# Performance work log

Measured on AMD Instinct MI355X. Metric: run time of the kernel, lower is better.

The kernel has to match this reference:

```python
import jax, jax.numpy as jnp
import numpy as np

N = 50000        # n_nodes
E = 1_600_000    # n_edges (avg degree 32)
IN = 128         # in_dim
H = 8            # num_heads
R = 16           # hidden_rank
D = 16           # out_dim (per head)
SCALE = float(np.sqrt(D))


def setup_inputs() -> dict:
    key = jax.random.key(0)
    k1, k2, k3, k4, k5, k6 = jax.random.split(key, 6)
    h = jax.random.normal(k1, (N, IN), jnp.float32)
    src = jax.random.randint(k2, (E,), 0, N, dtype=jnp.int32)
    dst = jax.random.randint(k3, (E,), 0, N, dtype=jnp.int32)
    s = 1.0 / np.sqrt(IN)  # kaiming-ish scale
    p = jax.random.normal(k4, (IN, H * R), jnp.float32) * s
    q = jax.random.normal(k5, (IN, H * R), jnp.float32) * s
    Wv = jax.random.normal(k6, (IN, H * D), jnp.float32) * s
    return {"h": h, "src": src, "dst": dst, "p": p, "q": q, "Wv": Wv}


def reference(h, src, dst, p, q, Wv):
    # global_attention_type == 'transform' -> atted = h
    K = (h @ q).reshape(N, H, R)   # K_h = atted @ _q
    Q = (h @ p).reshape(N, H, R)   # Q_h = h @ _p
    V = (h @ Wv).reshape(N, H, D)  # V_h = V(h), no bias
    # per-edge score: (K[src] * Q[dst]).sum(-1, keepdim), then scaled exp
    score = jnp.sum(K[src] * Q[dst], axis=-1, keepdims=True)   # [E, H, 1]
    score = jnp.exp(jnp.clip(score / SCALE, -5.0, 5.0))
    # scatter-sum into destination nodes
    wV = jax.ops.segment_sum(V[src] * score, dst, num_segments=N)  # [N, H, D]
    z = jax.ops.segment_sum(score, dst, num_segments=N)            # [N, H, 1]
    z = jnp.where(z == 0, jnp.float32(0.001), z)
    return wV / z
```

## Files before the change

### kernel.cpp

```cpp
#include <hip/hip_runtime.h>
#include <hip/hip_fp16.h>


#define HNODE 64
#define EPB   4096
#define BKT_SHIFT 7
#define BKT_CAP 5120
#define CHUNK 40

typedef _Float16 f16x8 __attribute__((ext_vector_type(8)));
typedef float    f32x4 __attribute__((ext_vector_type(4)));
typedef _Float16 hv2   __attribute__((ext_vector_type(2)));

__device__ __forceinline__ float fdot2(unsigned a, unsigned b, float c) {
#if __has_builtin(__builtin_amdgcn_fdot2)
    return __builtin_amdgcn_fdot2(__builtin_bit_cast(hv2, a),
                                  __builtin_bit_cast(hv2, b), c, false);
#else
    __half2 ah = *(__half2*)&a, bh = *(__half2*)&b;
    float2 af = __half22float2(ah), bf = __half22float2(bh);
    return c + af.x * bf.x + af.y * bf.y;
#endif
}

__device__ __forceinline__ float2 h2f(unsigned u) {
    __half2 hh = *(__half2*)&u;
    return __half22float2(hh);
}

__device__ __forceinline__ unsigned pack2(float a, float b) {
    __half2 hh = __floats2half2_rn(a, b);
    return *(unsigned*)&hh;
}

__device__ __forceinline__ float clamp5(float x) {
#if __has_builtin(__builtin_amdgcn_fmed3f)
    return __builtin_amdgcn_fmed3f(x, -5.f, 5.f);
#else
    return fminf(fmaxf(x, -5.f), 5.f);
#endif
}

#if __has_builtin(__builtin_amdgcn_mov_dpp)
#define QBCAST(v, J) __builtin_amdgcn_mov_dpp((v), (J) * 0x55, 0xF, 0xF, true)
__device__ __forceinline__ float qadd_xor1(float x) {
    int y = __builtin_amdgcn_mov_dpp(__float_as_int(x), 0xB1, 0xF, 0xF, true);
    return x + __int_as_float(y);
}
__device__ __forceinline__ float qadd_xor2(float x) {
    int y = __builtin_amdgcn_mov_dpp(__float_as_int(x), 0x4E, 0xF, 0xF, true);
    return x + __int_as_float(y);
}
#else
#define QBCAST(v, J) __shfl((v), ((threadIdx.x & 63) & ~3) + (J), 64)
__device__ __forceinline__ float qadd_xor1(float x) { return x + __shfl_xor(x, 1); }
__device__ __forceinline__ float qadd_xor2(float x) { return x + __shfl_xor(x, 2); }
#endif

__global__ __launch_bounds__(256) void wt_convert_kernel(
    const float* __restrict__ Wq, const float* __restrict__ Wp,
    const float* __restrict__ Wv, __half* __restrict__ Wt)
{
    int o = blockIdx.x * 256 + threadIdx.x;
    int m = o >> 14, rem = o & 16383;
    int nn = rem >> 7, kk = rem & 127;
    const float* W = (m == 0) ? Wq : (m == 1) ? Wp : Wv;
    Wt[o] = __float2half(W[kk * 128 + nn]);
}

__global__ __launch_bounds__(256) void gemm_scatter_kernel(
    const float* __restrict__ h, const __half* __restrict__ Wt,
    unsigned* __restrict__ KV, __half* __restrict__ Q, int n,
    const int* __restrict__ src, const int* __restrict__ dst,
    unsigned* __restrict__ ebuf, int* __restrict__ cnts,
    int E, int nbkt, int nblk_e, int gemm_blocks)
{
    __shared__ __align__(16) char smem[39936];
    const int t = threadIdx.x;

    if ((int)blockIdx.x < gemm_blocks) {
        _Float16* ws = (_Float16*)smem;
        const int wid = t >> 6, lane = t & 63;
        const int node0 = blockIdx.x * HNODE;
        const int mrow = lane & 15, quad = lane >> 4;

        const int row = node0 + wid * 16 + mrow;
        const bool rowvalid = (row < n);
        const int rowc = rowvalid ? row : (n - 1);

        f16x8 hfr[4];
        #pragma unroll
        for (int s = 0; s < 4; s++) {
            const float4* hp = (const float4*)(h + (size_t)rowc * 128 + quad * 8 + 32 * s);
            float4 f0 = hp[0], f1 = hp[1];
            f16x8 a;
            a[0] = (_Float16)f0.x; a[1] = (_Float16)f0.y;
            a[2] = (_Float16)f0.z; a[3] = (_Float16)f0.w;
            a[4] = (_Float16)f1.x; a[5] = (_Float16)f1.y;
            a[6] = (_Float16)f1.z; a[7] = (_Float16)f1.w;
            hfr[s] = a;
        }

        f32x4 acc[3][8];
        #pragma unroll
        for (int m = 0; m < 3; m++)
            #pragma unroll
            for (int ct = 0; ct < 8; ct++) acc[m][ct] = (f32x4){0.f, 0.f, 0.f, 0.f};

        #pragma unroll
        for (int m = 0; m < 3; m++) {
            __syncthreads();
            {
                const uint4* wg = (const uint4*)(Wt + (size_t)m * 16384);
                #pragma unroll
                for (int i = 0; i < 8; i++) {
                    int idx = t * 8 + i;
                    int r = idx >> 4, seg = idx & 15;
                    *(uint4*)(ws + r * 136 + seg * 8) = wg[idx];
                }
            }
            __syncthreads();
            #pragma unroll
            for (int s = 0; s < 4; s++) {
                #pragma unroll
                for (int ct = 0; ct < 8; ct++) {
                    f16x8 a = *(const f16x8*)(ws + (ct * 16 + mrow) * 136 + quad * 8 + 32 * s);
                    acc[m][ct] = __builtin_amdgcn_mfma_f32_16x16x32_f16(a, hfr[s], acc[m][ct], 0, 0, 0);
                }
            }
        }

        if (rowvalid) {
            #pragma unroll
            for (int ct = 0; ct < 8; ct++) {
                uint4 ov;
                ov.x = pack2(acc[0][ct][0], acc[0][ct][1]);
                ov.y = pack2(acc[0][ct][2], acc[0][ct][3]);
                ov.z = pack2(acc[2][ct][0], acc[2][ct][1]);
                ov.w = pack2(acc[2][ct][2], acc[2][ct][3]);
                *(uint4*)(KV + (((size_t)ct * n + row) << 4) + 4 * quad) = ov;
                uint2 qv;
                qv.x = pack2(acc[1][ct][0], acc[1][ct][1]);
                qv.y = pack2(acc[1][ct][2], acc[1][ct][3]);
                *(uint2*)(Q + (((size_t)ct * n + row) << 4) + 4 * quad) = qv;
            }
        }
    } else {
        unsigned long long* sorted = (unsigned long long*)smem;
        int* cnt  = (int*)(smem + 32768);
        int* lofs = (int*)(smem + 34816);
        int* ts   = (int*)(smem + 36864);
        int* tot_sh = (int*)(smem + 37888);

        int blk = blockIdx.x - gemm_blocks;
        for (int i = t; i < 512; i += 256) cnt[i] = 0;
        __syncthreads();

        int4 sv[4], dv[4], rk[4];
        int base = blk * EPB + t * 4;
        #pragma unroll
        for (int r = 0; r < 4; r++) {
            int i = base + r * 1024;
            if (i + 3 < E) {
                sv[r] = *(const int4*)(src + i);
                dv[r] = *(const int4*)(dst + i);
            } else {
                int tsrc[4], tdst[4];
                for (int k = 0; k < 4; k++) {
                    int j = i + k;
                    tsrc[k] = (j < E) ? src[j] : 0;
                    tdst[k] = (j < E) ? dst[j] : -1;
                }
                sv[r] = make_int4(tsrc[0], tsrc[1], tsrc[2], tsrc[3]);
                dv[r] = make_int4(tdst[0], tdst[1], tdst[2], tdst[3]);
            }
            rk[r].x = (dv[r].x >= 0) ? atomicAdd(&cnt[dv[r].x >> BKT_SHIFT], 1) : 0;
            rk[r].y = (dv[r].y >= 0) ? atomicAdd(&cnt[dv[r].y >> BKT_SHIFT], 1) : 0;
            rk[r].z = (dv[r].z >= 0) ? atomicAdd(&cnt[dv[r].z >> BKT_SHIFT], 1) : 0;
            rk[r].w = (dv[r].w >= 0) ? atomicAdd(&cnt[dv[r].w >> BKT_SHIFT], 1) : 0;
        }
        __syncthreads();

        for (int i = t; i < nbkt; i += 256)
            cnts[blk * 512 + i] = cnt[i];

        int c0 = cnt[2 * t], c1 = cnt[2 * t + 1];
        int ps = c0 + c1;
        ts[t] = ps; __syncthreads();
        for (int off = 1; off < 256; off <<= 1) {
            int x = ts[t];
            int y = (t >= off) ? ts[t - off] : 0;
            __syncthreads();
            ts[t] = x + y;
            __syncthreads();
        }
        int pbase = ts[t] - ps;
        lofs[2 * t] = pbase;
        lofs[2 * t + 1] = pbase + c0;
        if (t == 255) *tot_sh = ts[255];
        __syncthreads();

        #pragma unroll
        for (int r = 0; r < 4; r++) {
            int s, d;
            d = dv[r].x; if (d >= 0) { s = sv[r].x; sorted[lofs[d >> BKT_SHIFT] + rk[r].x] = ((unsigned long long)d << 18) | (unsigned)s; }
            d = dv[r].y; if (d >= 0) { s = sv[r].y; sorted[lofs[d >> BKT_SHIFT] + rk[r].y] = ((unsigned long long)d << 18) | (unsigned)s; }
            d = dv[r].z; if (d >= 0) { s = sv[r].z; sorted[lofs[d >> BKT_SHIFT] + rk[r].z] = ((unsigned long long)d << 18) | (unsigned)s; }
            d = dv[r].w; if (d >= 0) { s = sv[r].w; sorted[lofs[d >> BKT_SHIFT] + rk[r].w] = ((unsigned long long)d << 18) | (unsigned)s; }
        }
        __syncthreads();

        int tot = *tot_sh;
        #pragma unroll
        for (int j = 0; j < 16; j++) {
            int i = j * 256 + t;
            if (i < tot) {
                unsigned long long e = sorted[i];
                int d = (int)(e >> 18);
                int b = d >> BKT_SHIFT;
                int k = i - lofs[b];
                if (k < CHUNK)
                    ebuf[((size_t)b * nblk_e + blk) * CHUNK + k] =
                        ((unsigned)(d & 127) << 18) | (unsigned)(e & 0x3FFFFu);
            }
        }
    }
}

__global__ __launch_bounds__(512) void fine_scatter_kernel(
    const unsigned* __restrict__ ebuf, const int* __restrict__ cnts,
    int2* __restrict__ offs, unsigned short* __restrict__ csr,
    int* __restrict__ nodeord, int N, int nblk_e, int nbkt)
{
    __shared__ int cval[512];
    __shared__ int cofs[512];
    __shared__ int ts[512];
    __shared__ int ldeg[128];
    __shared__ int lstart[129];
    __shared__ int tot_sh;
    __shared__ unsigned sedge[BKT_CAP];
    __shared__ unsigned short srank[BKT_CAP];
    __shared__ int lcsr[BKT_CAP];

    int b = blockIdx.x, t = threadIdx.x;
    int node_base = b << BKT_SHIFT;
    int seg0 = b * BKT_CAP;

    int c = (t < nblk_e) ? cnts[t * 512 + b] : 0;
    if (c > CHUNK) c = CHUNK;
    cval[t] = c;
    ts[t] = c;
    if (t < 128) ldeg[t] = 0;
    __syncthreads();
    for (int off = 1; off < 512; off <<= 1) {
        int x = ts[t];
        int y = (t >= off) ? ts[t - off] : 0;
        __syncthreads();
        ts[t] = x + y;
        __syncthreads();
    }
    cofs[t] = ts[t] - cval[t];
    if (t == 511) tot_sh = (ts[511] <= BKT_CAP) ? ts[511] : BKT_CAP;
    __syncthreads();

    for (int idx = t; idx < nblk_e * CHUNK; idx += 512) {
        int cc = idx / CHUNK, k = idx - cc * CHUNK;
        if (k < cval[cc]) {
            int pos = cofs[cc] + k;
            if (pos < BKT_CAP)
                sedge[pos] = ebuf[((size_t)b * nblk_e + cc) * CHUNK + k];
        }
    }
    __syncthreads();

    int tot = tot_sh;
    for (int i = t; i < tot; i += 512)
        srank[i] = (unsigned short)atomicAdd(&ldeg[sedge[i] >> 18], 1);
    __syncthreads();

    int mydeg = (t < 128) ? ldeg[t] : 0;
    if (t < 128) ts[t] = mydeg;
    __syncthreads();
    for (int off = 1; off < 128; off <<= 1) {
        int x = (t < 128) ? ts[t] : 0;
        int y = (t >= off && t < 128) ? ts[t - off] : 0;
        __syncthreads();
        if (t < 128) ts[t] = x + y;
        __syncthreads();
    }
    if (t < 128) {
        int lbeg = ts[t] - mydeg;
        lstart[t] = lbeg;
        int node = node_base + t;
        if (node < N) offs[node] = make_int2(seg0 + lbeg, seg0 + lbeg + mydeg);
    }
    if (t == 127) lstart[128] = ts[127];
    __syncthreads();

    if (t < 128) {
        int dt = ldeg[t];
        int r = 0;
        for (int j = 0; j < 128; j++) {
            int dj = ldeg[j];
            r += (int)((dj > dt) || (dj == dt && j < t));
        }
        nodeord[(b << 7) + r] = t;
    }

    for (int i = t; i < tot; i += 512) {
        unsigned v = sedge[i];
        lcsr[lstart[v >> 18] + srank[i]] = (int)(v & 0x3FFFFu);
    }
    __syncthreads();

    for (int i = t; i < tot; i += 512)
        csr[seg0 + i] = (unsigned short)lcsr[i];
}

#define AGG_COMPUTE(A, J)                                                      \
    {                                                                          \
        float s = fdot2(A.x, qq.x, fdot2(A.y, qq.y, 0.f));                     \
        s = qadd_xor1(s);                                                      \
        s = qadd_xor2(s);                                                      \
        float xx = clamp5(s * 0.25f);                                          \
        float sc = (e + (J) < cnt) ? __expf(xx) : 0.f;                         \
        accz += sc;                                                            \
        float2 v0 = h2f(A.z), v1 = h2f(A.w);                                   \
        av0 += sc * v0.x; av1 += sc * v0.y;                                    \
        av2 += sc * v1.x; av3 += sc * v1.y;                                    \
    }

__global__ __launch_bounds__(256) void aggregate_kernel(
    const unsigned* __restrict__ KVh,
    const uint2* __restrict__ Qr,
    const int2* __restrict__ offs, const unsigned short* __restrict__ csr,
    const int* __restrict__ nodeord,
    float* __restrict__ out, int n)
{
    const int t = threadIdx.x;
    const int head = blockIdx.x & 7;
    const int rest = blockIdx.x >> 3;
    const int bkt = rest >> 1, sub = rest & 1;
    const int lane = t & 63;
    const int g = lane >> 2;
    const int p = lane & 3;
    const int chunk = ((t >> 6) << 1) | sub;

    const int spos = (bkt << 7) + (chunk << 4) + g;
    const int local = nodeord[spos];
    const int node = (bkt << 7) + local;
    const bool nvalid = (node < n);
    const int nodec = nvalid ? node : 0;

    int beg = 0, cnt = 0;
    if (nvalid) {
        int2 be = offs[node];
        beg = be.x; cnt = be.y - be.x;
    }

    const size_t hn = (size_t)head * n;
    const uint2 qq = Qr[(hn + nodec) * 4 + p];
    const char* kvb = (const char*)KVh + hn * 64;
    const unsigned ppo = (unsigned)p << 4;

    float accz = 0.f;
    float av0 = 0.f, av1 = 0.f, av2 = 0.f, av3 = 0.f;

    const int cl = (cnt > 0) ? (cnt - 1) : 0;

    int np = (p < cl) ? p : cl;
    int idxA = (int)csr[beg + np];
    uint4 a0, a1, a2, a3;
    {
        unsigned j;
        j = (unsigned)QBCAST(idxA, 0); a0 = *(const uint4*)(kvb + ((j << 6) | ppo));
        j = (unsigned)QBCAST(idxA, 1); a1 = *(const uint4*)(kvb + ((j << 6) | ppo));
        j = (unsigned)QBCAST(idxA, 2); a2 = *(const uint4*)(kvb + ((j << 6) | ppo));
        j = (unsigned)QBCAST(idxA, 3); a3 = *(const uint4*)(kvb + ((j << 6) | ppo));
    }
    np = 4 + p; np = (np < cl) ? np : cl;
    int idxB = (int)csr[beg + np];

    for (int e = 0; e < cnt; e += 4) {
        unsigned j;
        uint4 b0, b1, b2, b3;
        j = (unsigned)QBCAST(idxB, 0); b0 = *(const uint4*)(kvb + ((j << 6) | ppo));
        j = (unsigned)QBCAST(idxB, 1); b1 = *(const uint4*)(kvb + ((j << 6) | ppo));
        j = (unsigned)QBCAST(idxB, 2); b2 = *(const uint4*)(kvb + ((j << 6) | ppo));
        j = (unsigned)QBCAST(idxB, 3); b3 = *(const uint4*)(kvb + ((j << 6) | ppo));
        np = e + 8 + p; np = (np < cl) ? np : cl;
        idxB = (int)csr[beg + np];

        AGG_COMPUTE(a0, 0)
        AGG_COMPUTE(a1, 1)
        AGG_COMPUTE(a2, 2)
        AGG_COMPUTE(a3, 3)

        a0 = b0; a1 = b1; a2 = b2; a3 = b3;
    }

    if (nvalid) {
        float z = accz;
        if (z == 0.f) z = 0.001f;
        float inv = 1.0f / z;
        *(float4*)(out + (size_t)node * 128 + head * 16 + p * 4) =
            make_float4(av0 * inv, av1 * inv, av2 * inv, av3 * inv);
    }
}


extern "C" void kernel_launch(void* const* d_in, const int* in_sizes, int n_in,
                              void* d_out, int out_size, void* d_ws, size_t ws_size,
                              hipStream_t stream)
{
    const float* h   = (const float*)d_in[0];
    const int*   src = (const int*)d_in[1];
    const int*   dst = (const int*)d_in[2];
    const float* p   = (const float*)d_in[3];
    const float* q   = (const float*)d_in[4];
    const float* wv  = (const float*)d_in[5];
    float* out = (float*)d_out;

    const int N = in_sizes[0] / 128;
    const int E = in_sizes[1];
    const int nbkt = (N + 127) >> BKT_SHIFT;
    const int nblk_e = (E + EPB - 1) / EPB;
    const int gemm_blocks = (N + HNODE - 1) / HNODE;

    unsigned* KV = (unsigned*)d_ws;
    __half* Qh   = (__half*)(KV + (size_t)N * 128);
    unsigned* ebuf = (unsigned*)(Qh + (size_t)N * 128);
    int* cnts    = (int*)(ebuf + (size_t)nbkt * nblk_e * CHUNK);
    unsigned short* csr16 = (unsigned short*)(cnts + (size_t)nblk_e * 512);
    int2* offs   = (int2*)(csr16 + (size_t)nbkt * BKT_CAP);
    int* nodeord = (int*)(offs + N);
    __half* Wt   = (__half*)(nodeord + (size_t)nbkt * 128);

    wt_convert_kernel<<<192, 256, 0, stream>>>(q, p, wv, Wt);

    gemm_scatter_kernel<<<gemm_blocks + nblk_e, 256, 0, stream>>>(
        h, Wt, KV, Qh, N, src, dst, ebuf, cnts, E, nbkt, nblk_e, gemm_blocks);

    fine_scatter_kernel<<<nbkt, 512, 0, stream>>>(ebuf, cnts, offs, csr16, nodeord, N, nblk_e, nbkt);

    aggregate_kernel<<<nbkt * 16, 256, 0, stream>>>(
        KV, (const uint2*)Qh, offs, csr16, nodeord, (float*)out, N);
}
```

Baseline: 231.1 us.

## Replace two-level bucket sort with global-atomic degree count and direct placement

The CSR build no longer does a per-block local bucket sort into an intermediate edge buffer followed by a fine scatter kernel. It now counts per-node in-degrees with global atomics, computes per-node offsets and the degree ordering in a small kernel, and places each edge directly with a global atomic cursor. This drops the ebuf round trip and the heavy shared-memory sort, but adds a kernel launch, a second full read of src/dst, and 3.2M contended global atomics. The order of sources within each node's list becomes nondeterministic.

```diff
diff --git a/kernel.cpp b/kernel.cpp
--- a/kernel.cpp
+++ b/kernel.cpp
@@ -6,7 +6,6 @@
 #define EPB   4096
 #define BKT_SHIFT 7
 #define BKT_CAP 5120
-#define CHUNK 40
 
 typedef _Float16 f16x8 __attribute__((ext_vector_type(8)));
 typedef float    f32x4 __attribute__((ext_vector_type(4)));
@@ -59,23 +58,28 @@
 
 __global__ __launch_bounds__(256) void wt_convert_kernel(
     const float* __restrict__ Wq, const float* __restrict__ Wp,
-    const float* __restrict__ Wv, __half* __restrict__ Wt)
+    const float* __restrict__ Wv, __half* __restrict__ Wt,
+    int* __restrict__ deg, int N)
 {
     int o = blockIdx.x * 256 + threadIdx.x;
-    int m = o >> 14, rem = o & 16383;
-    int nn = rem >> 7, kk = rem & 127;
-    const float* W = (m == 0) ? Wq : (m == 1) ? Wp : Wv;
-    Wt[o] = __float2half(W[kk * 128 + nn]);
+    if (o < 49152) {
+        int m = o >> 14, rem = o & 16383;
+        int nn = rem >> 7, kk = rem & 127;
+        const float* W = (m == 0) ? Wq : (m == 1) ? Wp : Wv;
+        Wt[o] = __float2half(W[kk * 128 + nn]);
+    } else {
+        int i = o - 49152;
+        if (i < N) deg[i] = 0;
+    }
 }
 
 __global__ __launch_bounds__(256) void gemm_scatter_kernel(
     const float* __restrict__ h, const __half* __restrict__ Wt,
     unsigned* __restrict__ KV, __half* __restrict__ Q, int n,
-    const int* __restrict__ src, const int* __restrict__ dst,
-    unsigned* __restrict__ ebuf, int* __restrict__ cnts,
-    int E, int nbkt, int nblk_e, int gemm_blocks)
-{
-    __shared__ __align__(16) char smem[39936];
+    const int* __restrict__ dst, int* __restrict__ deg,
+    int E, int gemm_blocks)
+{
+    __shared__ __align__(16) char smem[34816];
     const int t = threadIdx.x;
 
     if ((int)blockIdx.x < gemm_blocks) {
@@ -146,175 +150,107 @@
             }
         }
     } else {
-        unsigned long long* sorted = (unsigned long long*)smem;
-        int* cnt  = (int*)(smem + 32768);
-        int* lofs = (int*)(smem + 34816);
-        int* ts   = (int*)(smem + 36864);
-        int* tot_sh = (int*)(smem + 37888);
-
         int blk = blockIdx.x - gemm_blocks;
-        for (int i = t; i < 512; i += 256) cnt[i] = 0;
-        __syncthreads();
-
-        int4 sv[4], dv[4], rk[4];
         int base = blk * EPB + t * 4;
         #pragma unroll
         for (int r = 0; r < 4; r++) {
             int i = base + r * 1024;
+            int4 dv;
             if (i + 3 < E) {
-                sv[r] = *(const int4*)(src + i);
-                dv[r] = *(const int4*)(dst + i);
+                dv = *(const int4*)(dst + i);
             } else {
-                int tsrc[4], tdst[4];
-                for (int k = 0; k < 4; k++) {
-                    int j = i + k;
-                    tsrc[k] = (j < E) ? src[j] : 0;
-                    tdst[k] = (j < E) ? dst[j] : -1;
-                }
-                sv[r] = make_int4(tsrc[0], tsrc[1], tsrc[2], tsrc[3]);
-                dv[r] = make_int4(tdst[0], tdst[1], tdst[2], tdst[3]);
+                dv.x = (i     < E) ? dst[i]     : -1;
+                dv.y = (i + 1 < E) ? dst[i + 1] : -1;
+                dv.z = (i + 2 < E) ? dst[i + 2] : -1;
+                dv.w = (i + 3 < E) ? dst[i + 3] : -1;
             }
-            rk[r].x = (dv[r].x >= 0) ? atomicAdd(&cnt[dv[r].x >> BKT_SHIFT], 1) : 0;
-            rk[r].y = (dv[r].y >= 0) ? atomicAdd(&cnt[dv[r].y >> BKT_SHIFT], 1) : 0;
-            rk[r].z = (dv[r].z >= 0) ? atomicAdd(&cnt[dv[r].z >> BKT_SHIFT], 1) : 0;
-            rk[r].w = (dv[r].w >= 0) ? atomicAdd(&cnt[dv[r].w >> BKT_SHIFT], 1) : 0;
-        }
-        __syncthreads();
-
-        for (int i = t; i < nbkt; i += 256)
-            cnts[blk * 512 + i] = cnt[i];
-
-        int c0 = cnt[2 * t], c1 = cnt[2 * t + 1];
-        int ps = c0 + c1;
-        ts[t] = ps; __syncthreads();
-        for (int off = 1; off < 256; off <<= 1) {
-            int x = ts[t];
-            int y = (t >= off) ? ts[t - off] : 0;
-            __syncthreads();
-            ts[t] = x + y;
-            __syncthreads();
-        }
-        int pbase = ts[t] - ps;
-        lofs[2 * t] = pbase;
-        lofs[2 * t + 1] = pbase + c0;
-        if (t == 255) *tot_sh = ts[255];
-        __syncthreads();
-
-        #pragma unroll
-        for (int r = 0; r < 4; r++) {
-            int s, d;
-            d = dv[r].x; if (d >= 0) { s = sv[r].x; sorted[lofs[d >> BKT_SHIFT] + rk[r].x] = ((unsigned long long)d << 18) | (unsigned)s; }
-            d = dv[r].y; if (d >= 0) { s = sv[r].y; sorted[lofs[d >> BKT_SHIFT] + rk[r].y] = ((unsigned long long)d << 18) | (unsigned)s; }
-            d = dv[r].z; if (d >= 0) { s = sv[r].z; sorted[lofs[d >> BKT_SHIFT] + rk[r].z] = ((unsigned long long)d << 18) | (unsigned)s; }
-            d = dv[r].w; if (d >= 0) { s = sv[r].w; sorted[lofs[d >> BKT_SHIFT] + rk[r].w] = ((unsigned long long)d << 18) | (unsigned)s; }
-        }
-        __syncthreads();
-
-        int tot = *tot_sh;
-        #pragma unroll
-        for (int j = 0; j < 16; j++) {
-            int i = j * 256 + t;
-            if (i < tot) {
-                unsigned long long e = sorted[i];
-                int d = (int)(e >> 18);
-                int b = d >> BKT_SHIFT;
-                int k = i - lofs[b];
-                if (k < CHUNK)
-                    ebuf[((size_t)b * nblk_e + blk) * CHUNK + k] =
-                        ((unsigned)(d & 127) << 18) | (unsigned)(e & 0x3FFFFu);
-            }
-        }
-    }
-}
-
-__global__ __launch_bounds__(512) void fine_scatter_kernel(
-    const unsigned* __restrict__ ebuf, const int* __restrict__ cnts,
-    int2* __restrict__ offs, unsigned short* __restrict__ csr,
-    int* __restrict__ nodeord, int N, int nblk_e, int nbkt)
-{
-    __shared__ int cval[512];
-    __shared__ int cofs[512];
-    __shared__ int ts[512];
-    __shared__ int ldeg[128];
-    __shared__ int lstart[129];
-    __shared__ int tot_sh;
-    __shared__ unsigned sedge[BKT_CAP];
-    __shared__ unsigned short srank[BKT_CAP];
-    __shared__ int lcsr[BKT_CAP];
-
+            if (dv.x >= 0) atomicAdd(&deg[dv.x], 1);
+            if (dv.y >= 0) atomicAdd(&deg[dv.y], 1);
+            if (dv.z >= 0) atomicAdd(&deg[dv.z], 1);
+            if (dv.w >= 0) atomicAdd(&deg[dv.w], 1);
+        }
+    }
+}
+
+__global__ __launch_bounds__(128) void bucket_offsets_kernel(
+    const int* __restrict__ deg, int2* __restrict__ offs,
+    int* __restrict__ cursor, int* __restrict__ nodeord, int N)
+{
+    __shared__ int sdeg[128];
+    __shared__ int ts[128];
     int b = blockIdx.x, t = threadIdx.x;
-    int node_base = b << BKT_SHIFT;
-    int seg0 = b * BKT_CAP;
-
-    int c = (t < nblk_e) ? cnts[t * 512 + b] : 0;
-    if (c > CHUNK) c = CHUNK;
-    cval[t] = c;
-    ts[t] = c;
-    if (t < 128) ldeg[t] = 0;
+    int node = (b << 7) + t;
+    int d = (node < N) ? deg[node] : 0;
+    sdeg[t] = d;
+    ts[t] = d;
     __syncthreads();
-    for (int off = 1; off < 512; off <<= 1) {
+    for (int off = 1; off < 128; off <<= 1) {
         int x = ts[t];
         int y = (t >= off) ? ts[t - off] : 0;
         __syncthreads();
         ts[t] = x + y;
         __syncthreads();
     }
-    cofs[t] = ts[t] - cval[t];
-    if (t == 511) tot_sh = (ts[511] <= BKT_CAP) ? ts[511] : BKT_CAP;
-    __syncthreads();
-
-    for (int idx = t; idx < nblk_e * CHUNK; idx += 512) {
-        int cc = idx / CHUNK, k = idx - cc * CHUNK;
-        if (k < cval[cc]) {
-            int pos = cofs[cc] + k;
-            if (pos < BKT_CAP)
-                sedge[pos] = ebuf[((size_t)b * nblk_e + cc) * CHUNK + k];
-        }
-    }
-    __syncthreads();
-
-    int tot = tot_sh;
-    for (int i = t; i < tot; i += 512)
-        srank[i] = (unsigned short)atomicAdd(&ldeg[sedge[i] >> 18], 1);
-    __syncthreads();
-
-    int mydeg = (t < 128) ? ldeg[t] : 0;
-    if (t < 128) ts[t] = mydeg;
-    __syncthreads();
-    for (int off = 1; off < 128; off <<= 1) {
-        int x = (t < 128) ? ts[t] : 0;
-        int y = (t >= off && t < 128) ? ts[t - off] : 0;
-        __syncthreads();
-        if (t < 128) ts[t] = x + y;
-        __syncthreads();
-    }
-    if (t < 128) {
-        int lbeg = ts[t] - mydeg;
-        lstart[t] = lbeg;
-        int node = node_base + t;
-        if (node < N) offs[node] = make_int2(seg0 + lbeg, seg0 + lbeg + mydeg);
-    }
-    if (t == 127) lstart[128] = ts[127];
-    __syncthreads();
-
-    if (t < 128) {
-        int dt = ldeg[t];
-        int r = 0;
-        for (int j = 0; j < 128; j++) {
-            int dj = ldeg[j];
-            r += (int)((dj > dt) || (dj == dt && j < t));
-        }
-        nodeord[(b << 7) + r] = t;
-    }
-
-    for (int i = t; i < tot; i += 512) {
-        unsigned v = sedge[i];
-        lcsr[lstart[v >> 18] + srank[i]] = (int)(v & 0x3FFFFu);
-    }
-    __syncthreads();
-
-    for (int i = t; i < tot; i += 512)
-        csr[seg0 + i] = (unsigned short)lcsr[i];
+    int pfx = ts[t] - d;
+    int seg0 = b * BKT_CAP;
+    if (node < N) {
+        offs[node] = make_int2(seg0 + pfx, seg0 + pfx + d);
+        cursor[node] = seg0 + pfx;
+    }
+    int r = 0;
+    #pragma unroll 8
+    for (int j = 0; j < 128; j++) {
+        int dj = sdeg[j];
+        r += (int)((dj > d) || (dj == d && j < t));
+    }
+    nodeord[(b << 7) + r] = t;
+}
+
+__global__ __launch_bounds__(256) void place_kernel(
+    const int* __restrict__ src, const int* __restrict__ dst,
+    int* __restrict__ cursor, unsigned short* __restrict__ csr, int E)
+{
+    const int t = threadIdx.x;
+    int base = blockIdx.x * EPB + t * 4;
+    #pragma unroll
+    for (int r = 0; r < 4; r++) {
+        int i = base + r * 1024;
+        int4 sv, dv;
+        if (i + 3 < E) {
+            sv = *(const int4*)(src + i);
+            dv = *(const int4*)(dst + i);
+        } else {
+            sv.x = (i     < E) ? src[i]     : 0;
+            sv.y = (i + 1 < E) ? src[i + 1] : 0;
+            sv.z = (i + 2 < E) ? src[i + 2] : 0;
+            sv.w = (i + 3 < E) ? src[i + 3] : 0;
+            dv.x = (i     < E) ? dst[i]     : -1;
+            dv.y = (i + 1 < E) ? dst[i + 1] : -1;
+            dv.z = (i + 2 < E) ? dst[i + 2] : -1;
+            dv.w = (i + 3 < E) ? dst[i + 3] : -1;
+        }
+        int pos, lim;
+        if (dv.x >= 0) {
+            pos = atomicAdd(&cursor[dv.x], 1);
+            lim = ((dv.x >> BKT_SHIFT) + 1) * BKT_CAP;
+            if (pos < lim) csr[pos] = (unsigned short)sv.x;
+        }
+        if (dv.y >= 0) {
+            pos = atomicAdd(&cursor[dv.y], 1);
+            lim = ((dv.y >> BKT_SHIFT) + 1) * BKT_CAP;
+            if (pos < lim) csr[pos] = (unsigned short)sv.y;
+        }
+        if (dv.z >= 0) {
+            pos = atomicAdd(&cursor[dv.z], 1);
+            lim = ((dv.z >> BKT_SHIFT) + 1) * BKT_CAP;
+            if (pos < lim) csr[pos] = (unsigned short)sv.z;
+        }
+        if (dv.w >= 0) {
+            pos = atomicAdd(&cursor[dv.w], 1);
+            lim = ((dv.w >> BKT_SHIFT) + 1) * BKT_CAP;
+            if (pos < lim) csr[pos] = (unsigned short)sv.w;
+        }
+    }
 }
 
 #define AGG_COMPUTE(A, J)                                                      \
@@ -429,19 +365,23 @@
 
     unsigned* KV = (unsigned*)d_ws;
     __half* Qh   = (__half*)(KV + (size_t)N * 128);
-    unsigned* ebuf = (unsigned*)(Qh + (size_t)N * 128);
-    int* cnts    = (int*)(ebuf + (size_t)nbkt * nblk_e * CHUNK);
-    unsigned short* csr16 = (unsigned short*)(cnts + (size_t)nblk_e * 512);
+    unsigned short* csr16 = (unsigned short*)(Qh + (size_t)N * 128);
     int2* offs   = (int2*)(csr16 + (size_t)nbkt * BKT_CAP);
     int* nodeord = (int*)(offs + N);
-    __half* Wt   = (__half*)(nodeord + (size_t)nbkt * 128);
-
-    wt_convert_kernel<<<192, 256, 0, stream>>>(q, p, wv, Wt);
+    int* deg     = nodeord + (size_t)nbkt * 128;
+    int* cursor  = deg + N;
+    __half* Wt   = (__half*)(cursor + N);
+
+    const int d0_blocks = 192 + (N + 255) / 256;
+
+    wt_convert_kernel<<<d0_blocks, 256, 0, stream>>>(q, p, wv, Wt, deg, N);
 
     gemm_scatter_kernel<<<gemm_blocks + nblk_e, 256, 0, stream>>>(
-        h, Wt, KV, Qh, N, src, dst, ebuf, cnts, E, nbkt, nblk_e, gemm_blocks);
-
-    fine_scatter_kernel<<<nbkt, 512, 0, stream>>>(ebuf, cnts, offs, csr16, nodeord, N, nblk_e, nbkt);
+        h, Wt, KV, Qh, N, dst, deg, E, gemm_blocks);
+
+    bucket_offsets_kernel<<<nbkt, 128, 0, stream>>>(deg, offs, cursor, nodeord, N);
+
+    place_kernel<<<nblk_e, 256, 0, stream>>>(src, dst, cursor, csr16, E);
 
     aggregate_kernel<<<nbkt * 16, 256, 0, stream>>>(
         KV, (const uint2*)Qh, offs, csr16, nodeord, (float*)out, N);
```

Result: slower. 360.4 us (+55.9%).

## Fuse per-bucket CSR construction into aggregate kernel using shared memory

Applied to the files above, without the earlier changes.

Removes the separate fine_scatter kernel and rebuilds each bucket's local CSR, degree-sorted node order and offsets in shared memory at the start of the aggregate kernel. This eliminates one launch and the global round trip for csr/offs/nodeord. Because each of the 8 head blocks per bucket now redoes the bucket sort, that work is repeated eightfold. Blocks grow to 512 threads with a large shared footprint, which may reduce occupancy for the gather loop.

```diff
diff --git a/kernel.cpp b/kernel.cpp
--- a/kernel.cpp
+++ b/kernel.cpp
@@ -227,96 +227,6 @@
     }
 }
 
-__global__ __launch_bounds__(512) void fine_scatter_kernel(
-    const unsigned* __restrict__ ebuf, const int* __restrict__ cnts,
-    int2* __restrict__ offs, unsigned short* __restrict__ csr,
-    int* __restrict__ nodeord, int N, int nblk_e, int nbkt)
-{
-    __shared__ int cval[512];
-    __shared__ int cofs[512];
-    __shared__ int ts[512];
-    __shared__ int ldeg[128];
-    __shared__ int lstart[129];
-    __shared__ int tot_sh;
-    __shared__ unsigned sedge[BKT_CAP];
-    __shared__ unsigned short srank[BKT_CAP];
-    __shared__ int lcsr[BKT_CAP];
-
-    int b = blockIdx.x, t = threadIdx.x;
-    int node_base = b << BKT_SHIFT;
-    int seg0 = b * BKT_CAP;
-
-    int c = (t < nblk_e) ? cnts[t * 512 + b] : 0;
-    if (c > CHUNK) c = CHUNK;
-    cval[t] = c;
-    ts[t] = c;
-    if (t < 128) ldeg[t] = 0;
-    __syncthreads();
-    for (int off = 1; off < 512; off <<= 1) {
-        int x = ts[t];
-        int y = (t >= off) ? ts[t - off] : 0;
-        __syncthreads();
-        ts[t] = x + y;
-        __syncthreads();
-    }
-    cofs[t] = ts[t] - cval[t];
-    if (t == 511) tot_sh = (ts[511] <= BKT_CAP) ? ts[511] : BKT_CAP;
-    __syncthreads();
-
-    for (int idx = t; idx < nblk_e * CHUNK; idx += 512) {
-        int cc = idx / CHUNK, k = idx - cc * CHUNK;
-        if (k < cval[cc]) {
-            int pos = cofs[cc] + k;
-            if (pos < BKT_CAP)
-                sedge[pos] = ebuf[((size_t)b * nblk_e + cc) * CHUNK + k];
-        }
-    }
-    __syncthreads();
-
-    int tot = tot_sh;
-    for (int i = t; i < tot; i += 512)
-        srank[i] = (unsigned short)atomicAdd(&ldeg[sedge[i] >> 18], 1);
-    __syncthreads();
-
-    int mydeg = (t < 128) ? ldeg[t] : 0;
-    if (t < 128) ts[t] = mydeg;
-    __syncthreads();
-    for (int off = 1; off < 128; off <<= 1) {
-        int x = (t < 128) ? ts[t] : 0;
-        int y = (t >= off && t < 128) ? ts[t - off] : 0;
-        __syncthreads();
-        if (t < 128) ts[t] = x + y;
-        __syncthreads();
-    }
-    if (t < 128) {
-        int lbeg = ts[t] - mydeg;
-        lstart[t] = lbeg;
-        int node = node_base + t;
-        if (node < N) offs[node] = make_int2(seg0 + lbeg, seg0 + lbeg + mydeg);
-    }
-    if (t == 127) lstart[128] = ts[127];
-    __syncthreads();
-
-    if (t < 128) {
-        int dt = ldeg[t];
-        int r = 0;
-        for (int j = 0; j < 128; j++) {
-            int dj = ldeg[j];
-            r += (int)((dj > dt) || (dj == dt && j < t));
-        }
-        nodeord[(b << 7) + r] = t;
-    }
-
-    for (int i = t; i < tot; i += 512) {
-        unsigned v = sedge[i];
-        lcsr[lstart[v >> 18] + srank[i]] = (int)(v & 0x3FFFFu);
-    }
-    __syncthreads();
-
-    for (int i = t; i < tot; i += 512)
-        csr[seg0 + i] = (unsigned short)lcsr[i];
-}
-
 #define AGG_COMPUTE(A, J)                                                      \
     {                                                                          \
         float s = fdot2(A.x, qq.x, fdot2(A.y, qq.y, 0.f));                     \
@@ -330,33 +240,98 @@
         av2 += sc * v1.x; av3 += sc * v1.y;                                    \
     }
 
-__global__ __launch_bounds__(256) void aggregate_kernel(
+__global__ __launch_bounds__(512) void aggregate_kernel(
     const unsigned* __restrict__ KVh,
     const uint2* __restrict__ Qr,
-    const int2* __restrict__ offs, const unsigned short* __restrict__ csr,
-    const int* __restrict__ nodeord,
-    float* __restrict__ out, int n)
+    const unsigned* __restrict__ ebuf, const int* __restrict__ cnts,
+    float* __restrict__ out, int n, int nblk_e)
 {
+    __shared__ int cval[512];
+    __shared__ int cofs[512];
+    __shared__ int ts[512];
+    __shared__ int ldeg[128];
+    __shared__ int lstart[128];
+    __shared__ unsigned char lord[128];
+    __shared__ int tot_sh;
+    __shared__ unsigned sedge[BKT_CAP];
+    __shared__ unsigned short srank[BKT_CAP];
+    __shared__ unsigned short lcsr[BKT_CAP];
+
     const int t = threadIdx.x;
     const int head = blockIdx.x & 7;
-    const int rest = blockIdx.x >> 3;
-    const int bkt = rest >> 1, sub = rest & 1;
+    const int b = blockIdx.x >> 3;
+
+    int c = (t < nblk_e) ? cnts[t * 512 + b] : 0;
+    if (c > CHUNK) c = CHUNK;
+    cval[t] = c;
+    ts[t] = c;
+    if (t < 128) ldeg[t] = 0;
+    __syncthreads();
+    for (int off = 1; off < 512; off <<= 1) {
+        int x = ts[t];
+        int y = (t >= off) ? ts[t - off] : 0;
+        __syncthreads();
+        ts[t] = x + y;
+        __syncthreads();
+    }
+    cofs[t] = ts[t] - cval[t];
+    if (t == 511) tot_sh = (ts[511] <= BKT_CAP) ? ts[511] : BKT_CAP;
+    __syncthreads();
+
+    for (int idx = t; idx < nblk_e * CHUNK; idx += 512) {
+        int cc = idx / CHUNK, k = idx - cc * CHUNK;
+        if (k < cval[cc]) {
+            int pos = cofs[cc] + k;
+            if (pos < BKT_CAP)
+                sedge[pos] = ebuf[((size_t)b * nblk_e + cc) * CHUNK + k];
+        }
+    }
+    __syncthreads();
+
+    const int tot = tot_sh;
+    for (int i = t; i < tot; i += 512)
+        srank[i] = (unsigned short)atomicAdd(&ldeg[sedge[i] >> 18], 1);
+    __syncthreads();
+
+    int mydeg = (t < 128) ? ldeg[t] : 0;
+    if (t < 128) ts[t] = mydeg;
+    __syncthreads();
+    for (int off = 1; off < 128; off <<= 1) {
+        int x = (t < 128) ? ts[t] : 0;
+        int y = (t >= off && t < 128) ? ts[t - off] : 0;
+        __syncthreads();
+        if (t < 128) ts[t] = x + y;
+        __syncthreads();
+    }
+    if (t < 128) {
+        lstart[t] = ts[t] - mydeg;
+        int r = 0;
+        for (int j = 0; j < 128; j++) {
+            int dj = ldeg[j];
+            r += (int)((dj > mydeg) || (dj == mydeg && j < t));
+        }
+        lord[r] = (unsigned char)t;
+    }
+    __syncthreads();
+
+    for (int i = t; i < tot; i += 512) {
+        unsigned v = sedge[i];
+        lcsr[lstart[v >> 18] + srank[i]] = (unsigned short)(v & 0x3FFFFu);
+    }
+    __syncthreads();
+
     const int lane = t & 63;
+    const int w = t >> 6;
     const int g = lane >> 2;
     const int p = lane & 3;
-    const int chunk = ((t >> 6) << 1) | sub;
-
-    const int spos = (bkt << 7) + (chunk << 4) + g;
-    const int local = nodeord[spos];
-    const int node = (bkt << 7) + local;
+
+    const int local = (int)lord[w * 16 + g];
+    const int node = (b << 7) + local;
     const bool nvalid = (node < n);
     const int nodec = nvalid ? node : 0;
 
-    int beg = 0, cnt = 0;
-    if (nvalid) {
-        int2 be = offs[node];
-        beg = be.x; cnt = be.y - be.x;
-    }
+    const int lbeg = lstart[local];
+    const int cnt = ldeg[local];
 
     const size_t hn = (size_t)head * n;
     const uint2 qq = Qr[(hn + nodec) * 4 + p];
@@ -369,7 +344,7 @@
     const int cl = (cnt > 0) ? (cnt - 1) : 0;
 
     int np = (p < cl) ? p : cl;
-    int idxA = (int)csr[beg + np];
+    int idxA = (int)lcsr[lbeg + np];
     uint4 a0, a1, a2, a3;
     {
         unsigned j;
@@ -379,7 +354,7 @@
         j = (unsigned)QBCAST(idxA, 3); a3 = *(const uint4*)(kvb + ((j << 6) | ppo));
     }
     np = 4 + p; np = (np < cl) ? np : cl;
-    int idxB = (int)csr[beg + np];
+    int idxB = (int)lcsr[lbeg + np];
 
     for (int e = 0; e < cnt; e += 4) {
         unsigned j;
@@ -389,7 +364,7 @@
         j = (unsigned)QBCAST(idxB, 2); b2 = *(const uint4*)(kvb + ((j << 6) | ppo));
         j = (unsigned)QBCAST(idxB, 3); b3 = *(const uint4*)(kvb + ((j << 6) | ppo));
         np = e + 8 + p; np = (np < cl) ? np : cl;
-        idxB = (int)csr[beg + np];
+        idxB = (int)lcsr[lbeg + np];
 
         AGG_COMPUTE(a0, 0)
         AGG_COMPUTE(a1, 1)
@@ -431,18 +406,13 @@
     __half* Qh   = (__half*)(KV + (size_t)N * 128);
     unsigned* ebuf = (unsigned*)(Qh + (size_t)N * 128);
     int* cnts    = (int*)(ebuf + (size_t)nbkt * nblk_e * CHUNK);
-    unsigned short* csr16 = (unsigned short*)(cnts + (size_t)nblk_e * 512);
-    int2* offs   = (int2*)(csr16 + (size_t)nbkt * BKT_CAP);
-    int* nodeord = (int*)(offs + N);
-    __half* Wt   = (__half*)(nodeord + (size_t)nbkt * 128);
+    __half* Wt   = (__half*)(cnts + (size_t)nblk_e * 512);
 
     wt_convert_kernel<<<192, 256, 0, stream>>>(q, p, wv, Wt);
 
     gemm_scatter_kernel<<<gemm_blocks + nblk_e, 256, 0, stream>>>(
         h, Wt, KV, Qh, N, src, dst, ebuf, cnts, E, nbkt, nblk_e, gemm_blocks);
 
-    fine_scatter_kernel<<<nbkt, 512, 0, stream>>>(ebuf, cnts, offs, csr16, nodeord, N, nblk_e, nbkt);
-
-    aggregate_kernel<<<nbkt * 16, 256, 0, stream>>>(
-        KV, (const uint2*)Qh, offs, csr16, nodeord, (float*)out, N);
-}
+    aggregate_kernel<<<nbkt * 8, 512, 0, stream>>>(
+        KV, (const uint2*)Qh, ebuf, cnts, (float*)out, N, nblk_e);
+}
```

Result: slower. 279.9 us (+21.1%).

## Replace per-block chunked edge buffer with atomic-reserved per-bucket global CSR

Applied to the files above, without the earlier changes.

The coarse scatter now reserves space in each destination bucket with a global atomicAdd on a per-bucket counter and writes edges straight into a contiguous per-bucket region. This replaces the fixed CHUNK-sized slots per (bucket, block) pair and the prefix scan over block counts. The fine kernel then reads one contiguous segment per bucket instead of gathering across 391 chunks, and it uses 16-bit local CSR staging. The per-bucket counters are zeroed in the weight-convert kernel. The cost is global atomic contention, and edge order within a bucket becomes nondeterministic, which can change floating-point summation order.

```diff
diff --git a/kernel.cpp b/kernel.cpp
--- a/kernel.cpp
+++ b/kernel.cpp
@@ -6,7 +6,6 @@
 #define EPB   4096
 #define BKT_SHIFT 7
 #define BKT_CAP 5120
-#define CHUNK 40
 
 typedef _Float16 f16x8 __attribute__((ext_vector_type(8)));
 typedef float    f32x4 __attribute__((ext_vector_type(4)));
@@ -59,21 +58,27 @@
 
 __global__ __launch_bounds__(256) void wt_convert_kernel(
     const float* __restrict__ Wq, const float* __restrict__ Wp,
-    const float* __restrict__ Wv, __half* __restrict__ Wt)
+    const float* __restrict__ Wv, __half* __restrict__ Wt,
+    int* __restrict__ btot, int nbkt)
 {
     int o = blockIdx.x * 256 + threadIdx.x;
-    int m = o >> 14, rem = o & 16383;
-    int nn = rem >> 7, kk = rem & 127;
-    const float* W = (m == 0) ? Wq : (m == 1) ? Wp : Wv;
-    Wt[o] = __float2half(W[kk * 128 + nn]);
+    if (o < 49152) {
+        int m = o >> 14, rem = o & 16383;
+        int nn = rem >> 7, kk = rem & 127;
+        const float* W = (m == 0) ? Wq : (m == 1) ? Wp : Wv;
+        Wt[o] = __float2half(W[kk * 128 + nn]);
+    } else {
+        int i = o - 49152;
+        if (i < nbkt) btot[i] = 0;
+    }
 }
 
 __global__ __launch_bounds__(256) void gemm_scatter_kernel(
     const float* __restrict__ h, const __half* __restrict__ Wt,
     unsigned* __restrict__ KV, __half* __restrict__ Q, int n,
     const int* __restrict__ src, const int* __restrict__ dst,
-    unsigned* __restrict__ ebuf, int* __restrict__ cnts,
-    int E, int nbkt, int nblk_e, int gemm_blocks)
+    unsigned* __restrict__ gcsr, int* __restrict__ btot,
+    int E, int nbkt, int gemm_blocks)
 {
     __shared__ __align__(16) char smem[39936];
     const int t = threadIdx.x;
@@ -150,7 +155,7 @@
         int* cnt  = (int*)(smem + 32768);
         int* lofs = (int*)(smem + 34816);
         int* ts   = (int*)(smem + 36864);
-        int* tot_sh = (int*)(smem + 37888);
+        int* base_sh = (int*)(smem + 37888);
 
         int blk = blockIdx.x - gemm_blocks;
         for (int i = t; i < 512; i += 256) cnt[i] = 0;
@@ -181,9 +186,6 @@
         }
         __syncthreads();
 
-        for (int i = t; i < nbkt; i += 256)
-            cnts[blk * 512 + i] = cnt[i];
-
         int c0 = cnt[2 * t], c1 = cnt[2 * t + 1];
         int ps = c0 + c1;
         ts[t] = ps; __syncthreads();
@@ -197,7 +199,11 @@
         int pbase = ts[t] - ps;
         lofs[2 * t] = pbase;
         lofs[2 * t + 1] = pbase + c0;
-        if (t == 255) *tot_sh = ts[255];
+
+        for (int i = t; i < nbkt; i += 256) {
+            int c = cnt[i];
+            base_sh[i] = (c > 0) ? atomicAdd(&btot[i], c) : 0;
+        }
         __syncthreads();
 
         #pragma unroll
@@ -210,7 +216,7 @@
         }
         __syncthreads();
 
-        int tot = *tot_sh;
+        int tot = ts[255];
         #pragma unroll
         for (int j = 0; j < 16; j++) {
             int i = j * 256 + t;
@@ -219,63 +225,42 @@
                 int d = (int)(e >> 18);
                 int b = d >> BKT_SHIFT;
                 int k = i - lofs[b];
-                if (k < CHUNK)
-                    ebuf[((size_t)b * nblk_e + blk) * CHUNK + k] =
+                int pos = base_sh[b] + k;
+                if (pos < BKT_CAP)
+                    gcsr[(size_t)b * BKT_CAP + pos] =
                         ((unsigned)(d & 127) << 18) | (unsigned)(e & 0x3FFFFu);
             }
         }
     }
 }
 
-__global__ __launch_bounds__(512) void fine_scatter_kernel(
-    const unsigned* __restrict__ ebuf, const int* __restrict__ cnts,
+__global__ __launch_bounds__(512) void fine2_kernel(
+    const unsigned* __restrict__ gcsr, const int* __restrict__ btot,
     int2* __restrict__ offs, unsigned short* __restrict__ csr,
-    int* __restrict__ nodeord, int N, int nblk_e, int nbkt)
+    int* __restrict__ nodeord, int N)
 {
-    __shared__ int cval[512];
-    __shared__ int cofs[512];
-    __shared__ int ts[512];
-    __shared__ int ldeg[128];
-    __shared__ int lstart[129];
-    __shared__ int tot_sh;
     __shared__ unsigned sedge[BKT_CAP];
     __shared__ unsigned short srank[BKT_CAP];
-    __shared__ int lcsr[BKT_CAP];
-
-    int b = blockIdx.x, t = threadIdx.x;
-    int node_base = b << BKT_SHIFT;
-    int seg0 = b * BKT_CAP;
-
-    int c = (t < nblk_e) ? cnts[t * 512 + b] : 0;
-    if (c > CHUNK) c = CHUNK;
-    cval[t] = c;
-    ts[t] = c;
+    __shared__ unsigned short lcsr[BKT_CAP];
+    __shared__ int ldeg[128];
+    __shared__ int lstart[128];
+    __shared__ int ts[128];
+
+    const int b = blockIdx.x, t = threadIdx.x;
+    const int seg0 = b * BKT_CAP;
+
+    int tot = btot[b];
+    if (tot > BKT_CAP) tot = BKT_CAP;
+
     if (t < 128) ldeg[t] = 0;
     __syncthreads();
-    for (int off = 1; off < 512; off <<= 1) {
-        int x = ts[t];
-        int y = (t >= off) ? ts[t - off] : 0;
-        __syncthreads();
-        ts[t] = x + y;
-        __syncthreads();
-    }
-    cofs[t] = ts[t] - cval[t];
-    if (t == 511) tot_sh = (ts[511] <= BKT_CAP) ? ts[511] : BKT_CAP;
-    __syncthreads();
-
-    for (int idx = t; idx < nblk_e * CHUNK; idx += 512) {
-        int cc = idx / CHUNK, k = idx - cc * CHUNK;
-        if (k < cval[cc]) {
-            int pos = cofs[cc] + k;
-            if (pos < BKT_CAP)
-                sedge[pos] = ebuf[((size_t)b * nblk_e + cc) * CHUNK + k];
-        }
-    }
-    __syncthreads();
-
-    int tot = tot_sh;
-    for (int i = t; i < tot; i += 512)
-        srank[i] = (unsigned short)atomicAdd(&ldeg[sedge[i] >> 18], 1);
+
+    const unsigned* gb = gcsr + (size_t)b * BKT_CAP;
+    for (int i = t; i < tot; i += 512) {
+        unsigned w = gb[i];
+        sedge[i] = w;
+        srank[i] = (unsigned short)atomicAdd(&ldeg[w >> 18], 1);
+    }
     __syncthreads();
 
     int mydeg = (t < 128) ? ldeg[t] : 0;
@@ -291,30 +276,25 @@
     if (t < 128) {
         int lbeg = ts[t] - mydeg;
         lstart[t] = lbeg;
-        int node = node_base + t;
+        int node = (b << 7) + t;
         if (node < N) offs[node] = make_int2(seg0 + lbeg, seg0 + lbeg + mydeg);
-    }
-    if (t == 127) lstart[128] = ts[127];
-    __syncthreads();
-
-    if (t < 128) {
-        int dt = ldeg[t];
         int r = 0;
         for (int j = 0; j < 128; j++) {
             int dj = ldeg[j];
-            r += (int)((dj > dt) || (dj == dt && j < t));
+            r += (int)((dj > mydeg) || (dj == mydeg && j < t));
         }
         nodeord[(b << 7) + r] = t;
     }
+    __syncthreads();
 
     for (int i = t; i < tot; i += 512) {
-        unsigned v = sedge[i];
-        lcsr[lstart[v >> 18] + srank[i]] = (int)(v & 0x3FFFFu);
+        unsigned w = sedge[i];
+        lcsr[lstart[w >> 18] + srank[i]] = (unsigned short)(w & 0x3FFFFu);
     }
     __syncthreads();
 
     for (int i = t; i < tot; i += 512)
-        csr[seg0 + i] = (unsigned short)lcsr[i];
+        csr[seg0 + i] = lcsr[i];
 }
 
 #define AGG_COMPUTE(A, J)                                                      \
@@ -429,19 +409,19 @@
 
     unsigned* KV = (unsigned*)d_ws;
     __half* Qh   = (__half*)(KV + (size_t)N * 128);
-    unsigned* ebuf = (unsigned*)(Qh + (size_t)N * 128);
-    int* cnts    = (int*)(ebuf + (size_t)nbkt * nblk_e * CHUNK);
-    unsigned short* csr16 = (unsigned short*)(cnts + (size_t)nblk_e * 512);
+    unsigned* gcsr = (unsigned*)(Qh + (size_t)N * 128);
+    int* btot    = (int*)(gcsr + (size_t)nbkt * BKT_CAP);
+    unsigned short* csr16 = (unsigned short*)(btot + 512);
     int2* offs   = (int2*)(csr16 + (size_t)nbkt * BKT_CAP);
     int* nodeord = (int*)(offs + N);
     __half* Wt   = (__half*)(nodeord + (size_t)nbkt * 128);
 
-    wt_convert_kernel<<<192, 256, 0, stream>>>(q, p, wv, Wt);
+    wt_convert_kernel<<<194, 256, 0, stream>>>(q, p, wv, Wt, btot, nbkt);
 
     gemm_scatter_kernel<<<gemm_blocks + nblk_e, 256, 0, stream>>>(
-        h, Wt, KV, Qh, N, src, dst, ebuf, cnts, E, nbkt, nblk_e, gemm_blocks);
-
-    fine_scatter_kernel<<<nbkt, 512, 0, stream>>>(ebuf, cnts, offs, csr16, nodeord, N, nblk_e, nbkt);
+        h, Wt, KV, Qh, N, src, dst, gcsr, btot, E, nbkt, gemm_blocks);
+
+    fine2_kernel<<<nbkt, 512, 0, stream>>>(gcsr, btot, offs, csr16, nodeord, N);
 
     aggregate_kernel<<<nbkt * 16, 256, 0, stream>>>(
         KV, (const uint2*)Qh, offs, csr16, nodeord, (float*)out, N);
```

Result: faster. 214.4 us (-7.3%).
